# Kernel tuning notes

Hardware: AMD Instinct MI355X
Metric: run time of the kernel (lower is better)

Reference implementation:

```python
import jax, jax.numpy as jnp
import numpy as np

D_MODEL = 768
N_HEADS = 12
D_HEAD = 64
N_MEM = 3072
ALPHA = 0.1
EPS = 1e-5
W_SCALE = 0.02  # standard init scale so energies/grads stay well-conditioned


def setup_inputs() -> dict:
    key = jax.random.key(0)
    k0, k1, k2, k3 = jax.random.split(key, 4)
    B, S = 8, 1024
    x = jax.random.normal(k0, (B, S, D_MODEL), jnp.float32)
    gamma = jnp.ones((1,), jnp.float32)                      # scalar LN gamma (ET uses a single gamma)
    delta = jnp.zeros((D_MODEL,), jnp.float32)               # LN bias
    Wq = jax.random.normal(k1, (N_HEADS, D_HEAD, D_MODEL), jnp.float32) * W_SCALE
    Wk = jax.random.normal(k2, (N_HEADS, D_HEAD, D_MODEL), jnp.float32) * W_SCALE
    beta = jnp.ones((N_HEADS,), jnp.float32) / np.sqrt(D_HEAD)  # per-head beta init 1/sqrt(d_head)
    xi = jax.random.normal(k3, (N_MEM, D_MODEL), jnp.float32) * W_SCALE
    return {"x": x, "gamma": gamma, "delta": delta, "Wq": Wq, "Wk": Wk,
            "beta": beta, "xi": xi, "n_steps": 12}


def _total_energy(x, gamma, delta, Wq, Wk, beta, xi):
    # --- EnergyLayerNorm: g = dL/dx, E_ln = <x, g> - L ---
    mean = jnp.mean(x, axis=-1, keepdims=True)
    xm = x - mean
    var = jnp.mean(xm * xm, axis=-1, keepdims=True)
    std = jnp.sqrt(var + EPS)
    g = gamma * xm / std + delta                       # (B,S,D)
    L = jnp.sum(D_MODEL * gamma * std) + jnp.sum(delta * x)
    e_ln = jnp.sum(x * g) - L
    # --- EnergyAttention: E = -sum_{b,h,q} (1/beta_h) * logsumexp_k(beta_h * Q.K) ---
    q = jnp.einsum('bsd,hyd->bhsy', g, Wq)
    k = jnp.einsum('bsd,hyd->bhsy', g, Wk)
    A = jnp.einsum('bhqy,bhky->bhqk', q, k)            # (B,H,S,S)
    lse = jax.nn.logsumexp(beta[None, :, None, None] * A, axis=-1)  # (B,H,S)
    e_attn = -jnp.sum(lse / beta[None, :, None])
    # --- HopfieldNetwork: E = -1/2 sum relu(g @ xi^T)^2 ---
    h = jnp.einsum('bsd,md->bsm', g, xi)               # (B,S,M)
    e_hop = -0.5 * jnp.sum(jnp.square(jax.nn.relu(h)))
    return e_ln + e_attn + e_hop


def reference(x, gamma, delta, Wq, Wk, beta, xi, n_steps):
    grad_fn = jax.grad(_total_energy, argnums=0)

    def step(state, _):
        return state - ALPHA * grad_fn(state, gamma, delta, Wq, Wk, beta, xi), None

    final, _ = jax.lax.scan(step, x, None, length=n_steps)
    return final
```

## Files before the change

### kernel.cpp

```cpp
#include <hip/hip_runtime.h>
#include <hip/hip_bf16.h>
#include <stdint.h>

#define T_TOK 8192
#define DM    768
#define NH    12
#define DH    64
#define SEQ   1024
#define NBH   96
#define NMEM  3072
#define NUP   4608
#define ALPHA 0.1f
#define EPS   1e-5f
#define NSTEPS 12
#define PAD   72
#define SPLITK 2

typedef unsigned short us;
typedef __bf16 bf16x8 __attribute__((ext_vector_type(8)));
typedef float  f32x4  __attribute__((ext_vector_type(4)));

__device__ __forceinline__ us f2bf(float f) {
  uint32_t u = __builtin_bit_cast(uint32_t, f);
  u += 0x7fffu + ((u >> 16) & 1u);
  return (us)(u >> 16);
}

__device__ __forceinline__ f32x4 mfma16(bf16x8 a, bf16x8 b, f32x4 c) {
  return __builtin_amdgcn_mfma_f32_16x16x32_bf16(a, b, c, 0, 0, 0);
}

__device__ __forceinline__ void gld16(const void* g, void* l) {
  __builtin_amdgcn_global_load_lds(
      (const __attribute__((address_space(1))) void*)(uintptr_t)g,
      (__attribute__((address_space(3))) void*)(uint32_t)(uintptr_t)l,
      16, 0, 0);
}

__device__ __forceinline__ float block_sum(float v, float* sb, int tid) {
#pragma unroll
  for (int d = 32; d >= 1; d >>= 1) v += __shfl_xor(v, d);
  __syncthreads();
  if ((tid & 63) == 0) sb[tid >> 6] = v;
  __syncthreads();
  return sb[0] + sb[1] + sb[2] + sb[3];
}

__global__ __launch_bounds__(256) void pack_w(const float* __restrict__ Wq,
                                              const float* __restrict__ Wk,
                                              const float* __restrict__ xi,
                                              us* __restrict__ Wup, us* __restrict__ WdT) {
  int idx = blockIdx.x * 256 + threadIdx.x;
  if (idx >= NUP * DM) return;
  int r = idx / DM, d = idx - r * DM;
  float v = (r < 768) ? Wq[idx] : (r < 1536 ? Wk[idx - 768 * DM] : xi[idx - 1536 * DM]);
  us h = f2bf(v);
  Wup[idx] = h;
  WdT[(size_t)d * NUP + r] = h;
}

__global__ __launch_bounds__(256) void ln_fwd(const float* __restrict__ X,
                                              const float* __restrict__ gamma,
                                              const float* __restrict__ delta,
                                              us* __restrict__ g_bf,
                                              float* __restrict__ meanb, float* __restrict__ rstdb) {
  int t = blockIdx.x, tid = threadIdx.x;
  const float* x = X + (size_t)t * DM;
  __shared__ float sb[4];
  float v0 = x[tid], v1 = x[tid + 256], v2 = x[tid + 512];
  float mean = block_sum(v0 + v1 + v2, sb, tid) * (1.0f / DM);
  float d0 = v0 - mean, d1 = v1 - mean, d2 = v2 - mean;
  float var = block_sum(d0 * d0 + d1 * d1 + d2 * d2, sb, tid) * (1.0f / DM);
  float rstd = rsqrtf(var + EPS);
  float gm = gamma[0];
  us* go = g_bf + (size_t)t * DM;
  go[tid]       = f2bf(gm * d0 * rstd + delta[tid]);
  go[tid + 256] = f2bf(gm * d1 * rstd + delta[tid + 256]);
  go[tid + 512] = f2bf(gm * d2 * rstd + delta[tid + 512]);
  if (tid == 0) { meanb[t] = mean; rstdb[t] = rstd; }
}

template <int MODE>
__global__ __launch_bounds__(256, 4) void gemm_bt(const us* __restrict__ A, const us* __restrict__ B,
                                                  int Kstride, int kchunk, us* __restrict__ QKout,
                                                  us* __restrict__ Dout, float* __restrict__ Gout) {
  __shared__ us As[2 * 128 * 32];
  __shared__ us Bs[2 * 128 * 32];
  int tid = threadIdx.x;
  int w = tid >> 6, lane = tid & 63, lm = lane & 15, lq = lane >> 4;
  int wm = (w >> 1) * 64, wn = (w & 1) * 64;

  int m0 = blockIdx.x * 128, n0 = blockIdx.y * 128;
  int kbeg = blockIdx.z * kchunk;
  int NT = kchunk >> 5;

  int sr  = tid >> 2;
  int k8s = (tid & 3) ^ ((tid >> 3) & 3);
  const us* pa = A + (size_t)(m0 + sr) * Kstride + kbeg + k8s * 8;
  const us* pb = B + (size_t)(n0 + sr) * Kstride + kbeg + k8s * 8;
  const size_t hstep = (size_t)64 * Kstride;
  us* dA0 = &As[tid * 8];
  us* dB0 = &Bs[tid * 8];

  int kx = (lq ^ ((lm >> 1) & 3)) * 8;
  const us* Ar = As + (wm + lm) * 32 + kx;
  const us* Br = Bs + (wn + lm) * 32 + kx;

  f32x4 zero4 = {0.f, 0.f, 0.f, 0.f};
  f32x4 acc[4][4];
#pragma unroll
  for (int i = 0; i < 4; i++)
#pragma unroll
    for (int j = 0; j < 4; j++) acc[i][j] = zero4;

#define STAGE(S, T) { gld16(pa + (size_t)(T) * 32,         dA0 + (S) * 4096);        \
                      gld16(pa + (size_t)(T) * 32 + hstep, dA0 + (S) * 4096 + 2048); \
                      gld16(pb + (size_t)(T) * 32,         dB0 + (S) * 4096);        \
                      gld16(pb + (size_t)(T) * 32 + hstep, dB0 + (S) * 4096 + 2048); }

  STAGE(0, 0);
  asm volatile("s_waitcnt vmcnt(0)" ::: "memory");
  __builtin_amdgcn_s_barrier();

#define ITER(T, S) {                                                            \
    if ((T) + 1 < NT) STAGE((S) ^ 1, (T) + 1);                                  \
    bf16x8 af_[4], bf_[4];                                                      \
    _Pragma("unroll") for (int x = 0; x < 4; x++)                               \
      af_[x] = *(const bf16x8*)(Ar + (S) * 4096 + x * 512);                     \
    _Pragma("unroll") for (int x = 0; x < 4; x++)                               \
      bf_[x] = *(const bf16x8*)(Br + (S) * 4096 + x * 512);                     \
    _Pragma("unroll") for (int mt = 0; mt < 4; mt++)                            \
      _Pragma("unroll") for (int nt = 0; nt < 4; nt++)                          \
        acc[mt][nt] = mfma16(bf_[nt], af_[mt], acc[mt][nt]);       \
    if ((T) + 1 < NT) {                                                         \
      asm volatile("s_waitcnt lgkmcnt(0)" ::: "memory");                        \
      asm volatile("s_waitcnt vmcnt(0)" ::: "memory");                          \
      __builtin_amdgcn_s_barrier();                                             \
    }                                                                           \
  }

  for (int t = 0; t < NT; t += 2) {
    ITER(t,     0);
    ITER(t + 1, 1);
  }
#undef ITER
#undef STAGE

  int cb = wn + lq * 4;
  if (MODE == 0 && n0 < 1536) {
#pragma unroll
    for (int mt = 0; mt < 4; mt++) {
      us* rowp = QKout + (size_t)(m0 + wm + mt * 16 + lm) * 1536 + n0 + cb;
#pragma unroll
      for (int nt = 0; nt < 4; nt++) {
        f32x4 v = acc[mt][nt];
        uint2 p;
        p.x = (uint32_t)f2bf(v[0]) | ((uint32_t)f2bf(v[1]) << 16);
        p.y = (uint32_t)f2bf(v[2]) | ((uint32_t)f2bf(v[3]) << 16);
        *(uint2*)(rowp + nt * 16) = p;
      }
    }
  } else if (MODE == 0) {
#pragma unroll
    for (int mt = 0; mt < 4; mt++) {
      us* rowp = Dout + (size_t)(m0 + wm + mt * 16 + lm) * NUP + n0 + cb;
#pragma unroll
      for (int nt = 0; nt < 4; nt++) {
        f32x4 v = acc[mt][nt];
        uint2 p;
        p.x = (uint32_t)f2bf(fmaxf(v[0], 0.f)) | ((uint32_t)f2bf(fmaxf(v[1], 0.f)) << 16);
        p.y = (uint32_t)f2bf(fmaxf(v[2], 0.f)) | ((uint32_t)f2bf(fmaxf(v[3], 0.f)) << 16);
        *(uint2*)(rowp + nt * 16) = p;
      }
    }
  } else {
    float* Gz = Gout + (size_t)blockIdx.z * T_TOK * DM;
#pragma unroll
    for (int mt = 0; mt < 4; mt++) {
      float* rowp = Gz + (size_t)(m0 + wm + mt * 16 + lm) * DM + n0 + cb;
#pragma unroll
      for (int nt = 0; nt < 4; nt++)
        *(f32x4*)(rowp + nt * 16) = acc[mt][nt];
    }
  }
}

__global__ __launch_bounds__(256) void transpose_qk(const us* __restrict__ QK,
                                                    us* __restrict__ Qt, us* __restrict__ Kt) {
  int bh = blockIdx.x, kt = blockIdx.y, which = blockIdx.z;
  int b = bh / NH, h = bh - b * NH;
  int tid = threadIdx.x;
  __shared__ us tile[64][72];
  int c0 = h * 64 + (which ? 768 : 0);
  us* dst = (which ? Kt : Qt) + (size_t)bh * 64 * 1024;
#pragma unroll
  for (int r = 0; r < 2; r++) {
    int key = r * 32 + (tid >> 3); int yb = (tid & 7) * 8;
    *(bf16x8*)&tile[key][yb] =
        *(const bf16x8*)&QK[(size_t)(b * SEQ + kt * 64 + key) * 1536 + c0 + yb];
  }
  __syncthreads();
#pragma unroll
  for (int r = 0; r < 2; r++) {
    int lin = r * 256 + tid; int y = lin >> 3; int kb = (lin & 7) * 8;
    __align__(16) us tmp[8];
#pragma unroll
    for (int j = 0; j < 8; j++) tmp[j] = tile[kb + j][y];
    *(bf16x8*)&dst[(size_t)y * 1024 + kt * 64 + kb] = *(bf16x8*)tmp;
  }
}

__global__ __launch_bounds__(256) void attn_fwd(const us* __restrict__ QK, const us* __restrict__ Ktg,
                                                const float* __restrict__ beta,
                                                us* __restrict__ Dbuf, float* __restrict__ lse) {
  __shared__ us Qs[64 * PAD];
  __shared__ us Ks[64 * PAD];
  __shared__ us Kts[64 * PAD];
  __shared__ us Ps[4 * 16 * PAD];
  int bh = blockIdx.x, qt = blockIdx.y;
  int b = bh / NH, h = bh - b * NH;
  int tid = threadIdx.x, w = tid >> 6, lane = tid & 63, lm = lane & 15, lq = lane >> 4;
  float betah = beta[h];
#pragma unroll
  for (int r = 0; r < 2; r++) {
    int row = r * 32 + (tid >> 3); int yb = (tid & 7) * 8;
    *(bf16x8*)&Qs[row * PAD + yb] =
        *(const bf16x8*)&QK[(size_t)(b * SEQ + qt * 64 + row) * 1536 + h * 64 + yb];
  }
  __syncthreads();
  bf16x8 aq0 = *(const bf16x8*)&Qs[(w * 16 + lm) * PAD + lq * 8];
  bf16x8 aq1 = *(const bf16x8*)&Qs[(w * 16 + lm) * PAD + 32 + lq * 8];
  f32x4 zero = {0.f, 0.f, 0.f, 0.f};
  f32x4 O[4] = {zero, zero, zero, zero};
  float lacc[4] = {0.f, 0.f, 0.f, 0.f};
  us* pw = &Ps[w * 16 * PAD];

  for (int kc = 0; kc < SEQ; kc += 64) {
    __syncthreads();
#pragma unroll
    for (int r = 0; r < 2; r++) {
      int row = r * 32 + (tid >> 3); int yb = (tid & 7) * 8;
      *(bf16x8*)&Ks[row * PAD + yb] =
          *(const bf16x8*)&QK[(size_t)(b * SEQ + kc + row) * 1536 + 768 + h * 64 + yb];
      int lin = r * 256 + tid; int y = lin >> 3; int kb = (lin & 7) * 8;
      *(bf16x8*)&Kts[y * PAD + kb] =
          *(const bf16x8*)&Ktg[(size_t)(bh * 64 + y) * 1024 + kc + kb];
    }
    __syncthreads();
#pragma unroll
    for (int kk = 0; kk < 4; kk++) {
      f32x4 s = mfma16(aq0, *(const bf16x8*)&Ks[(kk * 16 + lm) * PAD + lq * 8], zero);
      s = mfma16(aq1, *(const bf16x8*)&Ks[(kk * 16 + lm) * PAD + 32 + lq * 8], s);
#pragma unroll
      for (int r = 0; r < 4; r++) {
        float p = __expf(betah * s[r]);
        lacc[r] += p;
        pw[(lq * 4 + r) * PAD + kk * 16 + lm] = f2bf(p);
      }
    }
    bf16x8 pa0 = *(const bf16x8*)&pw[lm * PAD + lq * 8];
    bf16x8 pa1 = *(const bf16x8*)&pw[lm * PAD + 32 + lq * 8];
#pragma unroll
    for (int nt = 0; nt < 4; nt++) {
      O[nt] = mfma16(pa0, *(const bf16x8*)&Kts[(nt * 16 + lm) * PAD + lq * 8], O[nt]);
      O[nt] = mfma16(pa1, *(const bf16x8*)&Kts[(nt * 16 + lm) * PAD + 32 + lq * 8], O[nt]);
    }
  }
  float l[4];
#pragma unroll
  for (int r = 0; r < 4; r++) {
    float v = lacc[r];
    v += __shfl_xor(v, 1); v += __shfl_xor(v, 2);
    v += __shfl_xor(v, 4); v += __shfl_xor(v, 8);
    l[r] = v;
  }
  float inv[4];
#pragma unroll
  for (int r = 0; r < 4; r++) inv[r] = 1.f / l[r];
#pragma unroll
  for (int nt = 0; nt < 4; nt++)
#pragma unroll
    for (int r = 0; r < 4; r++) {
      int q = qt * 64 + w * 16 + lq * 4 + r;
      Dbuf[(size_t)(b * SEQ + q) * NUP + h * 64 + nt * 16 + lm] = f2bf(O[nt][r] * inv[r]);
    }
  if (lm == 0) {
#pragma unroll
    for (int r = 0; r < 4; r++)
      lse[bh * SEQ + qt * 64 + w * 16 + lq * 4 + r] = __logf(l[r]);
  }
}

__global__ __launch_bounds__(256) void attn_bwd(const us* __restrict__ QK, const us* __restrict__ Qtg,
                                                const float* __restrict__ lse,
                                                const float* __restrict__ beta,
                                                us* __restrict__ Dbuf) {
  __shared__ us Ks2[64 * PAD];
  __shared__ us Qs2[64 * PAD];
  __shared__ us Qts[64 * PAD];
  __shared__ us Ps[4 * 16 * PAD];
  int bh = blockIdx.x, kt = blockIdx.y;
  int b = bh / NH, h = bh - b * NH;
  int tid = threadIdx.x, w = tid >> 6, lane = tid & 63, lm = lane & 15, lq = lane >> 4;
  float betah = beta[h];
#pragma unroll
  for (int r = 0; r < 2; r++) {
    int row = r * 32 + (tid >> 3); int yb = (tid & 7) * 8;
    *(bf16x8*)&Ks2[row * PAD + yb] =
        *(const bf16x8*)&QK[(size_t)(b * SEQ + kt * 64 + row) * 1536 + 768 + h * 64 + yb];
  }
  __syncthreads();
  bf16x8 ak0 = *(const bf16x8*)&Ks2[(w * 16 + lm) * PAD + lq * 8];
  bf16x8 ak1 = *(const bf16x8*)&Ks2[(w * 16 + lm) * PAD + 32 + lq * 8];
  f32x4 zero = {0.f, 0.f, 0.f, 0.f};
  f32x4 O[4] = {zero, zero, zero, zero};
  us* pw = &Ps[w * 16 * PAD];

  for (int qc = 0; qc < SEQ; qc += 64) {
    __syncthreads();
#pragma unroll
    for (int r = 0; r < 2; r++) {
      int row = r * 32 + (tid >> 3); int yb = (tid & 7) * 8;
      *(bf16x8*)&Qs2[row * PAD + yb] =
          *(const bf16x8*)&QK[(size_t)(b * SEQ + qc + row) * 1536 + h * 64 + yb];
      int lin = r * 256 + tid; int y = lin >> 3; int qb = (lin & 7) * 8;
      *(bf16x8*)&Qts[y * PAD + qb] =
          *(const bf16x8*)&Qtg[(size_t)(bh * 64 + y) * 1024 + qc + qb];
    }
    __syncthreads();
#pragma unroll
    for (int kk = 0; kk < 4; kk++) {
      f32x4 s = mfma16(ak0, *(const bf16x8*)&Qs2[(kk * 16 + lm) * PAD + lq * 8], zero);
      s = mfma16(ak1, *(const bf16x8*)&Qs2[(kk * 16 + lm) * PAD + 32 + lq * 8], s);
      float lv = lse[bh * SEQ + qc + kk * 16 + lm];
#pragma unroll
      for (int r = 0; r < 4; r++)
        pw[(lq * 4 + r) * PAD + kk * 16 + lm] = f2bf(__expf(betah * s[r] - lv));
    }
    bf16x8 pa0 = *(const bf16x8*)&pw[lm * PAD + lq * 8];
    bf16x8 pa1 = *(const bf16x8*)&pw[lm * PAD + 32 + lq * 8];
#pragma unroll
    for (int nt = 0; nt < 4; nt++) {
      O[nt] = mfma16(pa0, *(const bf16x8*)&Qts[(nt * 16 + lm) * PAD + lq * 8], O[nt]);
      O[nt] = mfma16(pa1, *(const bf16x8*)&Qts[(nt * 16 + lm) * PAD + 32 + lq * 8], O[nt]);
    }
  }
#pragma unroll
  for (int nt = 0; nt < 4; nt++)
#pragma unroll
    for (int r = 0; r < 4; r++) {
      int key = kt * 64 + w * 16 + lq * 4 + r;
      Dbuf[(size_t)(b * SEQ + key) * NUP + 768 + h * 64 + nt * 16 + lm] = f2bf(O[nt][r]);
    }
}

__global__ __launch_bounds__(256) void update_x(float* __restrict__ X, const float* __restrict__ G,
                                                float* __restrict__ meanb,
                                                float* __restrict__ rstdb,
                                                const float* __restrict__ gamma,
                                                const float* __restrict__ delta,
                                                us* __restrict__ g_bf) {
  int t = blockIdx.x, tid = threadIdx.x;
  __shared__ float sb[4];
  float mean = meanb[t], rstd = rstdb[t], gm = gamma[0];
  float* x = X + (size_t)t * DM;
  const float* g0 = G + (size_t)t * DM;
  const size_t GS = (size_t)T_TOK * DM;
  int i0 = tid, i1 = tid + 256, i2 = tid + 512;
  float x0 = x[i0], x1 = x[i1], x2 = x[i2];
  float gv0 = 0.f, gv1 = 0.f, gv2 = 0.f;
#pragma unroll
  for (int z = 0; z < SPLITK; z++) {
    gv0 += g0[i0 + z * GS];
    gv1 += g0[i1 + z * GS];
    gv2 += g0[i2 + z * GS];
  }
  float v0 = x0 - gv0, v1 = x1 - gv1, v2 = x2 - gv2;
  float n0 = (x0 - mean) * rstd, n1 = (x1 - mean) * rstd, n2 = (x2 - mean) * rstd;
  float s1 = block_sum(v0 + v1 + v2, sb, tid) * (1.0f / DM);
  float s2 = block_sum(v0 * n0 + v1 * n1 + v2 * n2, sb, tid) * (1.0f / DM);
  float c = ALPHA * gm * rstd;
  float y0 = x0 - c * (v0 - s1 - n0 * s2);
  float y1 = x1 - c * (v1 - s1 - n1 * s2);
  float y2 = x2 - c * (v2 - s1 - n2 * s2);
  x[i0] = y0; x[i1] = y1; x[i2] = y2;
  float mean2 = block_sum(y0 + y1 + y2, sb, tid) * (1.0f / DM);
  float d0 = y0 - mean2, d1 = y1 - mean2, d2 = y2 - mean2;
  float var2 = block_sum(d0 * d0 + d1 * d1 + d2 * d2, sb, tid) * (1.0f / DM);
  float rstd2 = rsqrtf(var2 + EPS);
  us* go = g_bf + (size_t)t * DM;
  go[i0] = f2bf(gm * d0 * rstd2 + delta[i0]);
  go[i1] = f2bf(gm * d1 * rstd2 + delta[i1]);
  go[i2] = f2bf(gm * d2 * rstd2 + delta[i2]);
  if (tid == 0) { meanb[t] = mean2; rstdb[t] = rstd2; }
}

extern "C" void kernel_launch(void* const* d_in, const int* in_sizes, int n_in,
                              void* d_out, int out_size, void* d_ws, size_t ws_size,
                              hipStream_t stream) {
  const float* x_in  = (const float*)d_in[0];
  const float* gamma = (const float*)d_in[1];
  const float* delta = (const float*)d_in[2];
  const float* Wq    = (const float*)d_in[3];
  const float* Wk    = (const float*)d_in[4];
  const float* beta  = (const float*)d_in[5];
  const float* xi    = (const float*)d_in[6];
  float* X = (float*)d_out;

  char* p = (char*)d_ws;
  auto carve = [&](size_t bytes) -> char* {
    char* q = p; p += (bytes + 255) & ~(size_t)255; return q;
  };
  us*    g_bf  = (us*)carve((size_t)T_TOK * DM * 2);
  float* meanb = (float*)carve((size_t)T_TOK * 4);
  float* rstdb = (float*)carve((size_t)T_TOK * 4);
  us*    QK    = (us*)carve((size_t)T_TOK * 1536 * 2);
  float* G     = (float*)carve((size_t)SPLITK * T_TOK * DM * 4);
  us*    Qt    = (us*)G;
  us*    Kt    = Qt + (size_t)NBH * 64 * 1024;
  float* lseb  = (float*)carve((size_t)NBH * SEQ * 4);
  us*    Dbuf  = (us*)carve((size_t)T_TOK * NUP * 2);
  us*    Wup   = (us*)carve((size_t)NUP * DM * 2);
  us*    WdT   = (us*)carve((size_t)DM * NUP * 2);

  hipMemcpyAsync(X, x_in, (size_t)T_TOK * DM * 4, hipMemcpyDeviceToDevice, stream);
  pack_w<<<(NUP * DM + 255) / 256, 256, 0, stream>>>(Wq, Wk, xi, Wup, WdT);
  ln_fwd<<<T_TOK, 256, 0, stream>>>(X, gamma, delta, g_bf, meanb, rstdb);

  for (int s = 0; s < NSTEPS; s++) {
    gemm_bt<0><<<dim3(64, 36, 1), 256, 0, stream>>>(g_bf, Wup, DM, DM, QK, Dbuf, nullptr);
    transpose_qk<<<dim3(NBH, 16, 2), 256, 0, stream>>>(QK, Qt, Kt);
    attn_fwd<<<dim3(NBH, 16), 256, 0, stream>>>(QK, Kt, beta, Dbuf, lseb);
    attn_bwd<<<dim3(NBH, 16), 256, 0, stream>>>(QK, Qt, lseb, beta, Dbuf);
    gemm_bt<1><<<dim3(64, 6, SPLITK), 256, 0, stream>>>(Dbuf, WdT, NUP, NUP / SPLITK,
                                                        nullptr, nullptr, G);
    update_x<<<T_TOK, 256, 0, stream>>>(X, G, meanb, rstdb, gamma, delta, g_bf);
  }
}
```

Before: 3.544 ms.

## Process 128 query/key rows per block in attention kernels to reuse K/Q tiles

Each attn_fwd and attn_bwd block now owns 128 rows instead of 64, with each wave handling two 16-row sub-tiles per streamed 64-wide K (or Q) chunk. This halves the number of blocks and halves the global loads of the streamed K/Kt and Q/Qt tiles per unit of work. The cost is more registers per thread (two accumulator sets), a larger shared Q/K tile, and a grid of only 768 blocks, which reduces parallelism and latency hiding.

```diff
diff --git a/kernel.cpp b/kernel.cpp
--- a/kernel.cpp
+++ b/kernel.cpp
@@ -213,7 +213,7 @@
 __global__ __launch_bounds__(256) void attn_fwd(const us* __restrict__ QK, const us* __restrict__ Ktg,
                                                 const float* __restrict__ beta,
                                                 us* __restrict__ Dbuf, float* __restrict__ lse) {
-  __shared__ us Qs[64 * PAD];
+  __shared__ us Qs[128 * PAD];
   __shared__ us Ks[64 * PAD];
   __shared__ us Kts[64 * PAD];
   __shared__ us Ps[4 * 16 * PAD];
@@ -222,17 +222,25 @@
   int tid = threadIdx.x, w = tid >> 6, lane = tid & 63, lm = lane & 15, lq = lane >> 4;
   float betah = beta[h];
 #pragma unroll
-  for (int r = 0; r < 2; r++) {
+  for (int r = 0; r < 4; r++) {
     int row = r * 32 + (tid >> 3); int yb = (tid & 7) * 8;
     *(bf16x8*)&Qs[row * PAD + yb] =
-        *(const bf16x8*)&QK[(size_t)(b * SEQ + qt * 64 + row) * 1536 + h * 64 + yb];
+        *(const bf16x8*)&QK[(size_t)(b * SEQ + qt * 128 + row) * 1536 + h * 64 + yb];
   }
   __syncthreads();
-  bf16x8 aq0 = *(const bf16x8*)&Qs[(w * 16 + lm) * PAD + lq * 8];
-  bf16x8 aq1 = *(const bf16x8*)&Qs[(w * 16 + lm) * PAD + 32 + lq * 8];
+  bf16x8 aq0[2], aq1[2];
+#pragma unroll
+  for (int s = 0; s < 2; s++) {
+    aq0[s] = *(const bf16x8*)&Qs[(s * 64 + w * 16 + lm) * PAD + lq * 8];
+    aq1[s] = *(const bf16x8*)&Qs[(s * 64 + w * 16 + lm) * PAD + 32 + lq * 8];
+  }
   f32x4 zero = {0.f, 0.f, 0.f, 0.f};
-  f32x4 O[4] = {zero, zero, zero, zero};
-  float lacc[4] = {0.f, 0.f, 0.f, 0.f};
+  f32x4 O[2][4];
+  float lacc[2][4];
+#pragma unroll
+  for (int s = 0; s < 2; s++)
+#pragma unroll
+    for (int i = 0; i < 4; i++) { O[s][i] = zero; lacc[s][i] = 0.f; }
   us* pw = &Ps[w * 16 * PAD];
 
   for (int kc = 0; kc < SEQ; kc += 64) {
@@ -248,46 +256,52 @@
     }
     __syncthreads();
 #pragma unroll
-    for (int kk = 0; kk < 4; kk++) {
-      f32x4 s = mfma16(aq0, *(const bf16x8*)&Ks[(kk * 16 + lm) * PAD + lq * 8], zero);
-      s = mfma16(aq1, *(const bf16x8*)&Ks[(kk * 16 + lm) * PAD + 32 + lq * 8], s);
+    for (int s = 0; s < 2; s++) {
+#pragma unroll
+      for (int kk = 0; kk < 4; kk++) {
+        f32x4 sv = mfma16(aq0[s], *(const bf16x8*)&Ks[(kk * 16 + lm) * PAD + lq * 8], zero);
+        sv = mfma16(aq1[s], *(const bf16x8*)&Ks[(kk * 16 + lm) * PAD + 32 + lq * 8], sv);
+#pragma unroll
+        for (int r = 0; r < 4; r++) {
+          float p = __expf(betah * sv[r]);
+          lacc[s][r] += p;
+          pw[(lq * 4 + r) * PAD + kk * 16 + lm] = f2bf(p);
+        }
+      }
+      bf16x8 pa0 = *(const bf16x8*)&pw[lm * PAD + lq * 8];
+      bf16x8 pa1 = *(const bf16x8*)&pw[lm * PAD + 32 + lq * 8];
+#pragma unroll
+      for (int nt = 0; nt < 4; nt++) {
+        O[s][nt] = mfma16(pa0, *(const bf16x8*)&Kts[(nt * 16 + lm) * PAD + lq * 8], O[s][nt]);
+        O[s][nt] = mfma16(pa1, *(const bf16x8*)&Kts[(nt * 16 + lm) * PAD + 32 + lq * 8], O[s][nt]);
+      }
+    }
+  }
+#pragma unroll
+  for (int s = 0; s < 2; s++) {
+    float l[4];
+#pragma unroll
+    for (int r = 0; r < 4; r++) {
+      float v = lacc[s][r];
+      v += __shfl_xor(v, 1); v += __shfl_xor(v, 2);
+      v += __shfl_xor(v, 4); v += __shfl_xor(v, 8);
+      l[r] = v;
+    }
+    float inv[4];
+#pragma unroll
+    for (int r = 0; r < 4; r++) inv[r] = 1.f / l[r];
+#pragma unroll
+    for (int nt = 0; nt < 4; nt++)
 #pragma unroll
       for (int r = 0; r < 4; r++) {
-        float p = __expf(betah * s[r]);
-        lacc[r] += p;
-        pw[(lq * 4 + r) * PAD + kk * 16 + lm] = f2bf(p);
-      }
-    }
-    bf16x8 pa0 = *(const bf16x8*)&pw[lm * PAD + lq * 8];
-    bf16x8 pa1 = *(const bf16x8*)&pw[lm * PAD + 32 + lq * 8];
-#pragma unroll
-    for (int nt = 0; nt < 4; nt++) {
-      O[nt] = mfma16(pa0, *(const bf16x8*)&Kts[(nt * 16 + lm) * PAD + lq * 8], O[nt]);
-      O[nt] = mfma16(pa1, *(const bf16x8*)&Kts[(nt * 16 + lm) * PAD + 32 + lq * 8], O[nt]);
-    }
-  }
-  float l[4];
-#pragma unroll
-  for (int r = 0; r < 4; r++) {
-    float v = lacc[r];
-    v += __shfl_xor(v, 1); v += __shfl_xor(v, 2);
-    v += __shfl_xor(v, 4); v += __shfl_xor(v, 8);
-    l[r] = v;
-  }
-  float inv[4];
-#pragma unroll
-  for (int r = 0; r < 4; r++) inv[r] = 1.f / l[r];
-#pragma unroll
-  for (int nt = 0; nt < 4; nt++)
-#pragma unroll
-    for (int r = 0; r < 4; r++) {
-      int q = qt * 64 + w * 16 + lq * 4 + r;
-      Dbuf[(size_t)(b * SEQ + q) * NUP + h * 64 + nt * 16 + lm] = f2bf(O[nt][r] * inv[r]);
-    }
-  if (lm == 0) {
-#pragma unroll
-    for (int r = 0; r < 4; r++)
-      lse[bh * SEQ + qt * 64 + w * 16 + lq * 4 + r] = __logf(l[r]);
+        int q = qt * 128 + s * 64 + w * 16 + lq * 4 + r;
+        Dbuf[(size_t)(b * SEQ + q) * NUP + h * 64 + nt * 16 + lm] = f2bf(O[s][nt][r] * inv[r]);
+      }
+    if (lm == 0) {
+#pragma unroll
+      for (int r = 0; r < 4; r++)
+        lse[bh * SEQ + qt * 128 + s * 64 + w * 16 + lq * 4 + r] = __logf(l[r]);
+    }
   }
 }
 
@@ -295,7 +309,7 @@
                                                 const float* __restrict__ lse,
                                                 const float* __restrict__ beta,
                                                 us* __restrict__ Dbuf) {
-  __shared__ us Ks2[64 * PAD];
+  __shared__ us Ks2[128 * PAD];
   __shared__ us Qs2[64 * PAD];
   __shared__ us Qts[64 * PAD];
   __shared__ us Ps[4 * 16 * PAD];
@@ -304,16 +318,24 @@
   int tid = threadIdx.x, w = tid >> 6, lane = tid & 63, lm = lane & 15, lq = lane >> 4;
   float betah = beta[h];
 #pragma unroll
-  for (int r = 0; r < 2; r++) {
+  for (int r = 0; r < 4; r++) {
     int row = r * 32 + (tid >> 3); int yb = (tid & 7) * 8;
     *(bf16x8*)&Ks2[row * PAD + yb] =
-        *(const bf16x8*)&QK[(size_t)(b * SEQ + kt * 64 + row) * 1536 + 768 + h * 64 + yb];
+        *(const bf16x8*)&QK[(size_t)(b * SEQ + kt * 128 + row) * 1536 + 768 + h * 64 + yb];
   }
   __syncthreads();
-  bf16x8 ak0 = *(const bf16x8*)&Ks2[(w * 16 + lm) * PAD + lq * 8];
-  bf16x8 ak1 = *(const bf16x8*)&Ks2[(w * 16 + lm) * PAD + 32 + lq * 8];
+  bf16x8 ak0[2], ak1[2];
+#pragma unroll
+  for (int s = 0; s < 2; s++) {
+    ak0[s] = *(const bf16x8*)&Ks2[(s * 64 + w * 16 + lm) * PAD + lq * 8];
+    ak1[s] = *(const bf16x8*)&Ks2[(s * 64 + w * 16 + lm) * PAD + 32 + lq * 8];
+  }
   f32x4 zero = {0.f, 0.f, 0.f, 0.f};
-  f32x4 O[4] = {zero, zero, zero, zero};
+  f32x4 O[2][4];
+#pragma unroll
+  for (int s = 0; s < 2; s++)
+#pragma unroll
+    for (int i = 0; i < 4; i++) O[s][i] = zero;
   us* pw = &Ps[w * 16 * PAD];
 
   for (int qc = 0; qc < SEQ; qc += 64) {
@@ -329,29 +351,34 @@
     }
     __syncthreads();
 #pragma unroll
-    for (int kk = 0; kk < 4; kk++) {
-      f32x4 s = mfma16(ak0, *(const bf16x8*)&Qs2[(kk * 16 + lm) * PAD + lq * 8], zero);
-      s = mfma16(ak1, *(const bf16x8*)&Qs2[(kk * 16 + lm) * PAD + 32 + lq * 8], s);
-      float lv = lse[bh * SEQ + qc + kk * 16 + lm];
-#pragma unroll
-      for (int r = 0; r < 4; r++)
-        pw[(lq * 4 + r) * PAD + kk * 16 + lm] = f2bf(__expf(betah * s[r] - lv));
-    }
-    bf16x8 pa0 = *(const bf16x8*)&pw[lm * PAD + lq * 8];
-    bf16x8 pa1 = *(const bf16x8*)&pw[lm * PAD + 32 + lq * 8];
-#pragma unroll
-    for (int nt = 0; nt < 4; nt++) {
-      O[nt] = mfma16(pa0, *(const bf16x8*)&Qts[(nt * 16 + lm) * PAD + lq * 8], O[nt]);
-      O[nt] = mfma16(pa1, *(const bf16x8*)&Qts[(nt * 16 + lm) * PAD + 32 + lq * 8], O[nt]);
-    }
-  }
-#pragma unroll
-  for (int nt = 0; nt < 4; nt++)
-#pragma unroll
-    for (int r = 0; r < 4; r++) {
-      int key = kt * 64 + w * 16 + lq * 4 + r;
-      Dbuf[(size_t)(b * SEQ + key) * NUP + 768 + h * 64 + nt * 16 + lm] = f2bf(O[nt][r]);
-    }
+    for (int s = 0; s < 2; s++) {
+#pragma unroll
+      for (int kk = 0; kk < 4; kk++) {
+        f32x4 sv = mfma16(ak0[s], *(const bf16x8*)&Qs2[(kk * 16 + lm) * PAD + lq * 8], zero);
+        sv = mfma16(ak1[s], *(const bf16x8*)&Qs2[(kk * 16 + lm) * PAD + 32 + lq * 8], sv);
+        float lv = lse[bh * SEQ + qc + kk * 16 + lm];
+#pragma unroll
+        for (int r = 0; r < 4; r++)
+          pw[(lq * 4 + r) * PAD + kk * 16 + lm] = f2bf(__expf(betah * sv[r] - lv));
+      }
+      bf16x8 pa0 = *(const bf16x8*)&pw[lm * PAD + lq * 8];
+      bf16x8 pa1 = *(const bf16x8*)&pw[lm * PAD + 32 + lq * 8];
+#pragma unroll
+      for (int nt = 0; nt < 4; nt++) {
+        O[s][nt] = mfma16(pa0, *(const bf16x8*)&Qts[(nt * 16 + lm) * PAD + lq * 8], O[s][nt]);
+        O[s][nt] = mfma16(pa1, *(const bf16x8*)&Qts[(nt * 16 + lm) * PAD + 32 + lq * 8], O[s][nt]);
+      }
+    }
+  }
+#pragma unroll
+  for (int s = 0; s < 2; s++)
+#pragma unroll
+    for (int nt = 0; nt < 4; nt++)
+#pragma unroll
+      for (int r = 0; r < 4; r++) {
+        int key = kt * 128 + s * 64 + w * 16 + lq * 4 + r;
+        Dbuf[(size_t)(b * SEQ + key) * NUP + 768 + h * 64 + nt * 16 + lm] = f2bf(O[s][nt][r]);
+      }
 }
 
 __global__ __launch_bounds__(256) void update_x(float* __restrict__ X, const float* __restrict__ G,
@@ -430,8 +457,8 @@
   for (int s = 0; s < NSTEPS; s++) {
     gemm_bt<0><<<dim3(64, 36, 1), 256, 0, stream>>>(g_bf, Wup, DM, DM, QK, Dbuf, nullptr);
     transpose_qk<<<dim3(NBH, 16, 2), 256, 0, stream>>>(QK, Qt, Kt);
-    attn_fwd<<<dim3(NBH, 16), 256, 0, stream>>>(QK, Kt, beta, Dbuf, lseb);
-    attn_bwd<<<dim3(NBH, 16), 256, 0, stream>>>(QK, Qt, lseb, beta, Dbuf);
+    attn_fwd<<<dim3(NBH, 8), 256, 0, stream>>>(QK, Kt, beta, Dbuf, lseb);
+    attn_bwd<<<dim3(NBH, 8), 256, 0, stream>>>(QK, Qt, lseb, beta, Dbuf);
     gemm_bt<1><<<dim3(64, 6, SPLITK), 256, 0, stream>>>(Dbuf, WdT, NUP, NUP / SPLITK,
                                                         nullptr, nullptr, G);
     update_x<<<T_TOK, 256, 0, stream>>>(X, G, meanb, rstdb, gamma, delta, g_bf);
```

Result: slower. 3.737 ms (+5.4%).
